# Kernel optimization log

Hardware: AMD Instinct MI355X
Metric: run time of the kernel (lower is better)

The kernel has to match this reference:

```python
import jax, jax.numpy as jnp
import numpy as np

N, E, H, C = 10000, 160000, 7, 64
NEG_SLOPE = 0.2


def setup_inputs() -> dict:
    key = jax.random.key(0)
    ks = iter(jax.random.split(key, 32))
    def w(shape, fan_in):
        return jax.random.normal(next(ks), shape, jnp.float32) * (1.0 / np.sqrt(fan_in))
    inp = {
        "x": jax.random.normal(next(ks), (N, 1024), jnp.float32),
        "edge_index": jax.random.randint(next(ks), (2, E), 0, N, jnp.int64),
        # input MLP 1024->512->256->64
        "W1": w((1024, 512), 1024), "b1": jnp.zeros((512,), jnp.float32),
        "W2": w((512, 256), 512),   "b2": jnp.zeros((256,), jnp.float32),
        "W3": w((256, 64), 256),    "b3": jnp.zeros((64,), jnp.float32),
        # 5 stacked GATv2Conv(64,64,heads=7,concat=False) layers
        "Wl": w((5, 64, H * C), 64), "bl": jnp.zeros((5, H * C), jnp.float32),
        "Wr": w((5, 64, H * C), 64),
        "att": w((5, H, C), C),
        "cbias": jnp.zeros((5, C), jnp.float32),
        # output MLP 64->32->16->9
        "V1": w((64, 32), 64), "c1": jnp.zeros((32,), jnp.float32),
        "V2": w((32, 16), 32), "c2": jnp.zeros((16,), jnp.float32),
        "V3": w((16, 9), 16),  "c3": jnp.zeros((9,), jnp.float32),
    }
    return inp


def _gatv2_conv(x, src, dst, Wl, bl, Wr, att, bias):
    # x: [N,64]; src/dst: [E'] (self-loops already appended)
    xl = (x @ Wl + bl).reshape(N, H, C)   # lin_l (with bias)
    xr = (x @ Wr).reshape(N, H, C)        # lin_r (no bias)
    e = jax.nn.leaky_relu(xl[src] + xr[dst], NEG_SLOPE)      # [E',H,C]
    logits = jnp.einsum('ehc,hc->eh', e, att)                # [E',H]
    m = jax.ops.segment_max(logits, dst, num_segments=N)     # [N,H]
    a = jnp.exp(logits - m[dst])
    s = jax.ops.segment_sum(a, dst, num_segments=N)          # [N,H]
    alpha = a / (s[dst] + 1e-16)                             # ragged softmax per dst node
    out = jax.ops.segment_sum(alpha[:, :, None] * xl[src], dst, num_segments=N)  # [N,H,C]
    return out.mean(axis=1) + bias                           # concat=False -> mean heads


def reference(x, edge_index, W1, b1, W2, b2, W3, b3, Wl, bl, Wr, att, cbias,
              V1, c1, V2, c2, V3, c3):
    # GATv2Conv adds self-loops by default
    loops = jnp.arange(N, dtype=edge_index.dtype)
    src = jnp.concatenate([edge_index[0], loops])
    dst = jnp.concatenate([edge_index[1], loops])

    h = jax.nn.relu(x @ W1 + b1)
    h = jax.nn.relu(h @ W2 + b2)
    h = jax.nn.relu(h @ W3 + b3)
    for l in range(5):
        h = jax.nn.relu(_gatv2_conv(h, src, dst, Wl[l], bl[l], Wr[l], att[l], cbias[l]))
    h = jax.nn.relu(h) @ V1 + c1
    h = jax.nn.relu(h) @ V2 + c2
    h = jax.nn.relu(h) @ V3 + c3
    return jax.nn.log_softmax(h, axis=1)
```

## Files before the change

### kernel.cpp

```cpp
#include <hip/hip_runtime.h>
#include <hip/hip_bf16.h>
#include <math.h>

#define NNODES 10000
#define NEDGES 160000
#define ETOT (NEDGES + NNODES)
#define HEADS 7
#define CH 64
#define HC 448
#define HCP 1024

typedef __attribute__((ext_vector_type(8))) short short8;
typedef __attribute__((ext_vector_type(4))) float floatx4;

__device__ __forceinline__ float bf_lo(unsigned u) {
  return __uint_as_float(u << 16);
}
__device__ __forceinline__ float bf_hi(unsigned u) {
  return __uint_as_float(u & 0xffff0000u);
}
__device__ __forceinline__ short f2bf(float v) {
  return __bfloat16_as_short(__float2bfloat16(v));
}

#define P0 2560000
#define P1 (P0 + 512 * 1024)
#define P2 (P1 + 256 * 512)
#define P3 (P2 + 64 * 256)
#define P4 (P3 + 5 * HCP * 64)
#define P5 (P4 + 5 * HCP)
#define P6 (P5 + NNODES)
#define PTOT P6

__global__ __launch_bounds__(256) void prep_kernel(
    const float* __restrict__ x, short* __restrict__ xb,
    const float* __restrict__ W1, short* __restrict__ W1t,
    const float* __restrict__ W2, short* __restrict__ W2t,
    const float* __restrict__ W3, short* __restrict__ W3t,
    const float* __restrict__ Wl, const float* __restrict__ Wr,
    const float* __restrict__ bl, short* __restrict__ Wgt,
    float* __restrict__ bg, int* __restrict__ cnt) {
  int idx = blockIdx.x * 256 + threadIdx.x;
  if (idx < P0) {
    float4 v = *(const float4*)&x[(size_t)idx * 4];
    short4 o;
    o.x = f2bf(v.x); o.y = f2bf(v.y); o.z = f2bf(v.z); o.w = f2bf(v.w);
    *(short4*)&xb[(size_t)idx * 4] = o;
  } else if (idx < P1) {
    int i = idx - P0;
    int n = i / 1024, k = i % 1024;
    W1t[i] = f2bf(W1[(size_t)k * 512 + n]);
  } else if (idx < P2) {
    int i = idx - P1;
    int n = i / 512, k = i % 512;
    W2t[i] = f2bf(W2[(size_t)k * 256 + n]);
  } else if (idx < P3) {
    int i = idx - P2;
    int n = i / 256, k = i % 256;
    W3t[i] = f2bf(W3[(size_t)k * 64 + n]);
  } else if (idx < P4) {
    int i = idx - P3;
    int l = i / (HCP * 64);
    int rem = i % (HCP * 64);
    int col = rem / 64, k = rem % 64;
    int half = col >> 9;
    int within = col & 511;
    int c = within >> 3, h = within & 7;
    float v = 0.f;
    if (h < 7) {
      const float* W = half ? Wr : Wl;
      v = W[((size_t)l * 64 + k) * HC + h * 64 + c];
    }
    Wgt[i] = f2bf(v);
  } else if (idx < P5) {
    int i = idx - P4;
    int l = i >> 10, col = i & 1023;
    int half = col >> 9, within = col & 511;
    int c = within >> 3, h = within & 7;
    bg[i] = (!half && h < 7) ? bl[(size_t)l * HC + h * 64 + c] : 0.f;
  } else if (idx < P6) {
    cnt[idx - P5] = 1;
  }
}

template <int BM, int BN, int RELU>
__global__ __launch_bounds__(256) void mfma_gemm(
    const short* __restrict__ A, const short* __restrict__ Bt,
    const float* __restrict__ bias, short* __restrict__ C,
    int M, int K, int Nc) {
  __shared__ short As[BM * 64];
  __shared__ short Bs[BN * 64];
  constexpr int MI = BM / 32;
  constexpr int NJ = BN / 32;
  int tid = threadIdx.x;
  int lane = tid & 63, wave = tid >> 6;
  int wm = wave >> 1, wn = wave & 1;
  int row0 = blockIdx.x * BM, col0 = blockIdx.y * BN;
  floatx4 acc[MI][NJ] = {};

  for (int k0 = 0; k0 < K; k0 += 64) {
    #pragma unroll
    for (int i = 0; i < BM / 32; ++i) {
      int c = i * 4 + wave;
      int r = c * 8 + (lane >> 3);
      int k = (lane & 7) * 8;
      int grow = row0 + r;
      if (grow >= M) grow = M - 1;
      __builtin_amdgcn_global_load_lds(
          (const __attribute__((address_space(1))) void*)(A + (size_t)grow * K + k0 + k),
          (__attribute__((address_space(3))) void*)(As + c * 512), 16, 0, 0);
    }
    #pragma unroll
    for (int i = 0; i < BN / 32; ++i) {
      int c = i * 4 + wave;
      int r = c * 8 + (lane >> 3);
      int k = (lane & 7) * 8;
      int gcol = col0 + r;
      if (gcol >= Nc) gcol = Nc - 1;
      __builtin_amdgcn_global_load_lds(
          (const __attribute__((address_space(1))) void*)(Bt + (size_t)gcol * K + k0 + k),
          (__attribute__((address_space(3))) void*)(Bs + c * 512), 16, 0, 0);
    }
    __syncthreads();
    int lr = lane & 15, lq = lane >> 4;
    #pragma unroll
    for (int kk = 0; kk < 64; kk += 32) {
      short8 af[MI], bf[NJ];
      #pragma unroll
      for (int i = 0; i < MI; ++i)
        af[i] = *(const short8*)&As[(wm * (BM / 2) + i * 16 + lr) * 64 + kk + lq * 8];
      #pragma unroll
      for (int j = 0; j < NJ; ++j)
        bf[j] = *(const short8*)&Bs[(wn * (BN / 2) + j * 16 + lr) * 64 + kk + lq * 8];
      #pragma unroll
      for (int i = 0; i < MI; ++i)
        #pragma unroll
        for (int j = 0; j < NJ; ++j)
          acc[i][j] = __builtin_amdgcn_mfma_f32_16x16x32_bf16(
              af[i], bf[j], acc[i][j], 0, 0, 0);
    }
    __syncthreads();
  }

  int lr = lane & 15, lq = lane >> 4;
  #pragma unroll
  for (int j = 0; j < NJ; ++j) {
    int col = col0 + wn * (BN / 2) + j * 16 + lr;
    float bj = bias ? bias[col] : 0.f;
    #pragma unroll
    for (int i = 0; i < MI; ++i) {
      int rbase = row0 + wm * (BM / 2) + i * 16 + lq * 4;
      #pragma unroll
      for (int r = 0; r < 4; ++r) {
        int row = rbase + r;
        if (row < M) {
          float v = acc[i][j][r] + bj;
          if (RELU) v = fmaxf(v, 0.f);
          C[(size_t)row * Nc + col] = f2bf(v);
        }
      }
    }
  }
}

__global__ void hist_kernel(const int* __restrict__ ei, int* __restrict__ cnt) {
  int e = blockIdx.x * 256 + threadIdx.x;
  if (e < NEDGES) atomicAdd(&cnt[ei[NEDGES + e]], 1);
}

__global__ __launch_bounds__(1024) void scan_kernel(
    const int* __restrict__ cnt, int* __restrict__ row_start,
    int* __restrict__ cursor) {
  __shared__ int wsum[16];
  int t = threadIdx.x;
  int lane = t & 63, w = t >> 6;
  int base = t * 10;
  int v[10], s = 0;
  #pragma unroll
  for (int i = 0; i < 10; ++i) {
    v[i] = (base + i < NNODES) ? cnt[base + i] : 0;
    s += v[i];
  }
  int incl = s;
  #pragma unroll
  for (int off = 1; off < 64; off <<= 1) {
    int o = __shfl_up(incl, off, 64);
    if (lane >= off) incl += o;
  }
  if (lane == 63) wsum[w] = incl;
  __syncthreads();
  if (w == 0) {
    int wv = (lane < 16) ? wsum[lane] : 0;
    #pragma unroll
    for (int off = 1; off < 16; off <<= 1) {
      int o = __shfl_up(wv, off, 64);
      if (lane >= off) wv += o;
    }
    if (lane < 16) wsum[lane] = wv;
  }
  __syncthreads();
  int woff = (w > 0) ? wsum[w - 1] : 0;
  int excl = woff + incl - s;
  #pragma unroll
  for (int i = 0; i < 10; ++i) {
    if (base + i < NNODES) {
      row_start[base + i] = excl;
      cursor[base + i] = excl;
    }
    excl += v[i];
  }
  if (t == 1023) row_start[NNODES] = wsum[15];
}

__global__ void scatter_kernel(const int* __restrict__ ei,
                               int* __restrict__ cursor,
                               int* __restrict__ csr_src,
                               int* __restrict__ csr_dst) {
  int t = blockIdx.x * 256 + threadIdx.x;
  if (t < NNODES) {
    int pos = atomicAdd(&cursor[t], 1);
    csr_src[pos] = t;
    csr_dst[pos] = t;
  } else if (t < ETOT) {
    int e = t - NNODES;
    int d = ei[NEDGES + e];
    int pos = atomicAdd(&cursor[d], 1);
    csr_src[pos] = ei[e];
    csr_dst[pos] = d;
  }
}

__global__ __launch_bounds__(256) void edge_logits_kernel(
    const short* __restrict__ xlt, const float* __restrict__ att,
    const int* __restrict__ csr_src, const int* __restrict__ csr_dst,
    float* __restrict__ wbuf) {
  __shared__ float att_s[512];
  for (int i = threadIdx.x; i < 512; i += 256) {
    int c = i >> 3, h = i & 7;
    att_s[i] = (h < 7) ? att[h * 64 + c] : 0.f;
  }
  __syncthreads();
  int lane = threadIdx.x & 63;
  int wid = threadIdx.x >> 6;
  int eo = lane >> 3, cl = lane & 7;
  int e = (blockIdx.x * 4 + wid) * 8 + eo;
  int ec = (e < ETOT) ? e : (ETOT - 1);
  int s = csr_src[ec], d = csr_dst[ec];
  const uint4* xlp = (const uint4*)(xlt + (size_t)s * HCP);
  const uint4* xrp = (const uint4*)(xlt + (size_t)d * HCP + 512);
  float acc[7];
  #pragma unroll
  for (int h = 0; h < 7; ++h) acc[h] = 0.f;
  #pragma unroll
  for (int q = 0; q < 8; ++q) {
    int c = q * 8 + cl;
    uint4 a = xlp[c];
    uint4 b = xrp[c];
    float4 t0 = *(const float4*)&att_s[c * 8];
    float4 t1 = *(const float4*)&att_s[c * 8 + 4];
    float e0 = bf_lo(a.x) + bf_lo(b.x);
    float e1 = bf_hi(a.x) + bf_hi(b.x);
    float e2 = bf_lo(a.y) + bf_lo(b.y);
    float e3 = bf_hi(a.y) + bf_hi(b.y);
    float e4 = bf_lo(a.z) + bf_lo(b.z);
    float e5 = bf_hi(a.z) + bf_hi(b.z);
    float e6 = bf_lo(a.w) + bf_lo(b.w);
    e0 = fmaxf(e0, 0.2f * e0); e1 = fmaxf(e1, 0.2f * e1);
    e2 = fmaxf(e2, 0.2f * e2); e3 = fmaxf(e3, 0.2f * e3);
    e4 = fmaxf(e4, 0.2f * e4); e5 = fmaxf(e5, 0.2f * e5);
    e6 = fmaxf(e6, 0.2f * e6);
    acc[0] += t0.x * e0; acc[1] += t0.y * e1;
    acc[2] += t0.z * e2; acc[3] += t0.w * e3;
    acc[4] += t1.x * e4; acc[5] += t1.y * e5;
    acc[6] += t1.z * e6;
  }
  #pragma unroll
  for (int h = 0; h < 7; ++h) {
    acc[h] += __shfl_xor(acc[h], 1, 64);
    acc[h] += __shfl_xor(acc[h], 2, 64);
    acc[h] += __shfl_xor(acc[h], 4, 64);
  }
  float res = 0.f;
  #pragma unroll
  for (int h = 0; h < 7; ++h) res = (cl == h) ? acc[h] : res;
  float wv = (cl < 7) ? __expf(res) : 0.f;
  if (e < ETOT) wbuf[(size_t)e * 8 + cl] = wv;
}

template <int FINAL>
__global__ __launch_bounds__(256) void gat_agg2_kernel(
    const short* __restrict__ xlt, const float* __restrict__ wbuf,
    const float* __restrict__ cbias, const int* __restrict__ row_start,
    const int* __restrict__ csr_src, short* __restrict__ hout,
    const float* __restrict__ V1, const float* __restrict__ c1,
    const float* __restrict__ V2, const float* __restrict__ c2,
    const float* __restrict__ V3, const float* __restrict__ c3,
    float* __restrict__ out) {
  __shared__ float part[2][14][64];
  __shared__ float hb[2][64], r1[2][32], r2[2][16], z3[2][9];
  int lane = threadIdx.x & 63;
  int wv = threadIdx.x >> 6;
  int nw = wv >> 1;
  int half = wv & 1;
  int n = blockIdx.x * 2 + nw;
  int beg = row_start[n], end = row_start[n + 1];

  float o0 = 0.f, o1 = 0.f, o2 = 0.f, o3 = 0.f, o4 = 0.f, o5 = 0.f, o6 = 0.f;
  float s0 = 0.f, s1 = 0.f, s2 = 0.f, s3 = 0.f, s4 = 0.f, s5 = 0.f, s6 = 0.f;
  #pragma unroll 2
  for (int e = beg + half; e < end; e += 2) {
    int src = csr_src[e];
    float4 wa = *(const float4*)&wbuf[(size_t)e * 8];
    float4 wb = *(const float4*)&wbuf[(size_t)e * 8 + 4];
    uint4 xv = *(const uint4*)(xlt + (size_t)src * HCP + (size_t)lane * 8);
    o0 += wa.x * bf_lo(xv.x);
    o1 += wa.y * bf_hi(xv.x);
    o2 += wa.z * bf_lo(xv.y);
    o3 += wa.w * bf_hi(xv.y);
    o4 += wb.x * bf_lo(xv.z);
    o5 += wb.y * bf_hi(xv.z);
    o6 += wb.z * bf_lo(xv.w);
    s0 += wa.x; s1 += wa.y; s2 += wa.z; s3 += wa.w;
    s4 += wb.x; s5 += wb.y; s6 += wb.z;
  }

  if (half == 1) {
    part[nw][0][lane] = o0;  part[nw][1][lane] = o1;
    part[nw][2][lane] = o2;  part[nw][3][lane] = o3;
    part[nw][4][lane] = o4;  part[nw][5][lane] = o5;
    part[nw][6][lane] = o6;
    part[nw][7][lane] = s0;  part[nw][8][lane] = s1;
    part[nw][9][lane] = s2;  part[nw][10][lane] = s3;
    part[nw][11][lane] = s4; part[nw][12][lane] = s5;
    part[nw][13][lane] = s6;
  }
  __syncthreads();
  if (half == 0) {
    o0 += part[nw][0][lane];  o1 += part[nw][1][lane];
    o2 += part[nw][2][lane];  o3 += part[nw][3][lane];
    o4 += part[nw][4][lane];  o5 += part[nw][5][lane];
    o6 += part[nw][6][lane];
    s0 += part[nw][7][lane];  s1 += part[nw][8][lane];
    s2 += part[nw][9][lane];  s3 += part[nw][10][lane];
    s4 += part[nw][11][lane]; s5 += part[nw][12][lane];
    s6 += part[nw][13][lane];
    float accv = o0 / (s0 + 1e-16f) + o1 / (s1 + 1e-16f) + o2 / (s2 + 1e-16f) +
                 o3 / (s3 + 1e-16f) + o4 / (s4 + 1e-16f) + o5 / (s5 + 1e-16f) +
                 o6 / (s6 + 1e-16f);
    float v = fmaxf(accv * (1.0f / 7.0f) + cbias[lane], 0.f);
    if (!FINAL) {
      hout[(size_t)n * 64 + lane] = f2bf(v);
    } else {
      int t = lane;
      hb[nw][t] = v;
      if (t < 32) {
        float a = c1[t];
        #pragma unroll
        for (int k = 0; k < 64; ++k) a += hb[nw][k] * V1[k * 32 + t];
        r1[nw][t] = fmaxf(a, 0.f);
      }
      if (t < 16) {
        float a = c2[t];
        #pragma unroll
        for (int k = 0; k < 32; ++k) a += r1[nw][k] * V2[k * 16 + t];
        r2[nw][t] = fmaxf(a, 0.f);
      }
      if (t < 9) {
        float a = c3[t];
        #pragma unroll
        for (int k = 0; k < 16; ++k) a += r2[nw][k] * V3[k * 9 + t];
        z3[nw][t] = a;
      }
      if (t < 9) {
        float mx = z3[nw][0];
        #pragma unroll
        for (int k = 1; k < 9; ++k) mx = fmaxf(mx, z3[nw][k]);
        float s = 0.f;
        #pragma unroll
        for (int k = 0; k < 9; ++k) s += __expf(z3[nw][k] - mx);
        out[(size_t)n * 9 + t] = z3[nw][t] - mx - logf(s);
      }
    }
  }
}

extern "C" void kernel_launch(void* const* d_in, const int* in_sizes, int n_in,
                              void* d_out, int out_size, void* d_ws, size_t ws_size,
                              hipStream_t stream) {
  const float* x   = (const float*)d_in[0];
  const int*   ei  = (const int*)d_in[1];
  const float* W1  = (const float*)d_in[2];
  const float* b1  = (const float*)d_in[3];
  const float* W2  = (const float*)d_in[4];
  const float* b2  = (const float*)d_in[5];
  const float* W3  = (const float*)d_in[6];
  const float* b3  = (const float*)d_in[7];
  const float* Wl  = (const float*)d_in[8];
  const float* bl  = (const float*)d_in[9];
  const float* Wr  = (const float*)d_in[10];
  const float* att = (const float*)d_in[11];
  const float* cb  = (const float*)d_in[12];
  const float* V1  = (const float*)d_in[13];
  const float* c1  = (const float*)d_in[14];
  const float* V2  = (const float*)d_in[15];
  const float* c2  = (const float*)d_in[16];
  const float* V3  = (const float*)d_in[17];
  const float* c3  = (const float*)d_in[18];
  float* out = (float*)d_out;

  char* ws = (char*)d_ws;
  size_t off = 0;
  auto alloc = [&](size_t bytes) {
    void* p = ws + off;
    off = (off + bytes + 255) & ~(size_t)255;
    return p;
  };
  char* region0 = (char*)alloc((size_t)NNODES * 1024 * 2 + 1024);
  short* xb  = (short*)region0;
  short* h2  = (short*)region0;
  short* xlt = (short*)region0;
  char* region1 = (char*)alloc((size_t)NNODES * 512 * 2 + 1024);
  short* h1 = (short*)region1;
  short* hA = (short*)region1;
  short* hB = hA + (size_t)NNODES * 64;
  short* W1t = (short*)alloc((size_t)512 * 1024 * 2);
  short* W2t = (short*)alloc((size_t)256 * 512 * 2);
  short* W3t = (short*)alloc((size_t)64 * 256 * 2);
  short* Wgt = (short*)alloc((size_t)5 * HCP * 64 * 2);
  float* bg  = (float*)alloc((size_t)5 * HCP * 4);
  int* cnt       = (int*)alloc((size_t)NNODES * 4);
  int* row_start = (int*)alloc((size_t)(NNODES + 1) * 4);
  int* cursor    = (int*)alloc((size_t)NNODES * 4);
  int* csr_src   = (int*)alloc((size_t)ETOT * 4);
  int* csr_dst   = (int*)alloc((size_t)ETOT * 4);
  float* wbuf    = (float*)alloc((size_t)ETOT * 8 * 4);

  prep_kernel<<<(PTOT + 255) / 256, 256, 0, stream>>>(
      x, xb, W1, W1t, W2, W2t, W3, W3t, Wl, Wr, bl, Wgt, bg, cnt);

  hist_kernel<<<(NEDGES + 255) / 256, 256, 0, stream>>>(ei, cnt);
  scan_kernel<<<1, 1024, 0, stream>>>(cnt, row_start, cursor);
  scatter_kernel<<<(ETOT + 255) / 256, 256, 0, stream>>>(ei, cursor, csr_src, csr_dst);

  mfma_gemm<64, 128, 1><<<dim3(157, 4), 256, 0, stream>>>(
      xb, W1t, b1, h1, NNODES, 1024, 512);
  mfma_gemm<64, 128, 1><<<dim3(157, 2), 256, 0, stream>>>(
      h1, W2t, b2, h2, NNODES, 512, 256);
  mfma_gemm<64, 64, 1><<<dim3(157, 1), 256, 0, stream>>>(
      h2, W3t, b3, hA, NNODES, 256, 64);

  short* hcur = hA;
  short* hnext = hB;
  for (int layer = 0; layer < 5; ++layer) {
    mfma_gemm<128, 128, 0><<<dim3(79, 8), 256, 0, stream>>>(
        hcur, Wgt + (size_t)layer * HCP * 64, bg + (size_t)layer * HCP, xlt,
        NNODES, 64, HCP);
    edge_logits_kernel<<<(ETOT + 31) / 32, 256, 0, stream>>>(
        xlt, att + (size_t)layer * HC, csr_src, csr_dst, wbuf);
    if (layer < 4) {
      gat_agg2_kernel<0><<<5000, 256, 0, stream>>>(
          xlt, wbuf, cb + (size_t)layer * 64, row_start, csr_src, hnext,
          V1, c1, V2, c2, V3, c3, out);
    } else {
      gat_agg2_kernel<1><<<5000, 256, 0, stream>>>(
          xlt, wbuf, cb + (size_t)layer * 64, row_start, csr_src, hnext,
          V1, c1, V2, c2, V3, c3, out);
    }
    short* tmp = hcur; hcur = hnext; hnext = tmp;
  }
}
```

Before: 551.7 us.

## Fuse edge-logit computation into per-node GAT aggregation kernel

Merges the separate edge-logits kernel into the aggregation kernel. Each block now computes exp-logits for its two destination nodes' edges in chunks of up to 128, keeping the xr rows, attention weights and source indices in shared memory. This removes the global wbuf and csr_dst buffers, one kernel launch per layer, and the global write and read of edge weights. In exchange each block now runs the logit phase and the aggregation phase one after the other with barriers between them, and the logit phase may use threads poorly when degrees are low.

```diff
diff --git a/kernel.cpp b/kernel.cpp
--- a/kernel.cpp
+++ b/kernel.cpp
@@ -9,6 +9,7 @@
 #define CH 64
 #define HC 448
 #define HCP 1024
+#define CAP 128
 
 typedef __attribute__((ext_vector_type(8))) short short8;
 typedef __attribute__((ext_vector_type(4))) float floatx4;
@@ -214,128 +215,155 @@
 
 __global__ void scatter_kernel(const int* __restrict__ ei,
                                int* __restrict__ cursor,
-                               int* __restrict__ csr_src,
-                               int* __restrict__ csr_dst) {
+                               int* __restrict__ csr_src) {
   int t = blockIdx.x * 256 + threadIdx.x;
   if (t < NNODES) {
     int pos = atomicAdd(&cursor[t], 1);
     csr_src[pos] = t;
-    csr_dst[pos] = t;
   } else if (t < ETOT) {
     int e = t - NNODES;
     int d = ei[NEDGES + e];
     int pos = atomicAdd(&cursor[d], 1);
     csr_src[pos] = ei[e];
-    csr_dst[pos] = d;
-  }
-}
-
-__global__ __launch_bounds__(256) void edge_logits_kernel(
+  }
+}
+
+template <int FINAL>
+__global__ __launch_bounds__(256) void gat_layer_kernel(
     const short* __restrict__ xlt, const float* __restrict__ att,
-    const int* __restrict__ csr_src, const int* __restrict__ csr_dst,
-    float* __restrict__ wbuf) {
-  __shared__ float att_s[512];
-  for (int i = threadIdx.x; i < 512; i += 256) {
-    int c = i >> 3, h = i & 7;
-    att_s[i] = (h < 7) ? att[h * 64 + c] : 0.f;
-  }
-  __syncthreads();
-  int lane = threadIdx.x & 63;
-  int wid = threadIdx.x >> 6;
-  int eo = lane >> 3, cl = lane & 7;
-  int e = (blockIdx.x * 4 + wid) * 8 + eo;
-  int ec = (e < ETOT) ? e : (ETOT - 1);
-  int s = csr_src[ec], d = csr_dst[ec];
-  const uint4* xlp = (const uint4*)(xlt + (size_t)s * HCP);
-  const uint4* xrp = (const uint4*)(xlt + (size_t)d * HCP + 512);
-  float acc[7];
-  #pragma unroll
-  for (int h = 0; h < 7; ++h) acc[h] = 0.f;
-  #pragma unroll
-  for (int q = 0; q < 8; ++q) {
-    int c = q * 8 + cl;
-    uint4 a = xlp[c];
-    uint4 b = xrp[c];
-    float4 t0 = *(const float4*)&att_s[c * 8];
-    float4 t1 = *(const float4*)&att_s[c * 8 + 4];
-    float e0 = bf_lo(a.x) + bf_lo(b.x);
-    float e1 = bf_hi(a.x) + bf_hi(b.x);
-    float e2 = bf_lo(a.y) + bf_lo(b.y);
-    float e3 = bf_hi(a.y) + bf_hi(b.y);
-    float e4 = bf_lo(a.z) + bf_lo(b.z);
-    float e5 = bf_hi(a.z) + bf_hi(b.z);
-    float e6 = bf_lo(a.w) + bf_lo(b.w);
-    e0 = fmaxf(e0, 0.2f * e0); e1 = fmaxf(e1, 0.2f * e1);
-    e2 = fmaxf(e2, 0.2f * e2); e3 = fmaxf(e3, 0.2f * e3);
-    e4 = fmaxf(e4, 0.2f * e4); e5 = fmaxf(e5, 0.2f * e5);
-    e6 = fmaxf(e6, 0.2f * e6);
-    acc[0] += t0.x * e0; acc[1] += t0.y * e1;
-    acc[2] += t0.z * e2; acc[3] += t0.w * e3;
-    acc[4] += t1.x * e4; acc[5] += t1.y * e5;
-    acc[6] += t1.z * e6;
-  }
-  #pragma unroll
-  for (int h = 0; h < 7; ++h) {
-    acc[h] += __shfl_xor(acc[h], 1, 64);
-    acc[h] += __shfl_xor(acc[h], 2, 64);
-    acc[h] += __shfl_xor(acc[h], 4, 64);
-  }
-  float res = 0.f;
-  #pragma unroll
-  for (int h = 0; h < 7; ++h) res = (cl == h) ? acc[h] : res;
-  float wv = (cl < 7) ? __expf(res) : 0.f;
-  if (e < ETOT) wbuf[(size_t)e * 8 + cl] = wv;
-}
-
-template <int FINAL>
-__global__ __launch_bounds__(256) void gat_agg2_kernel(
-    const short* __restrict__ xlt, const float* __restrict__ wbuf,
     const float* __restrict__ cbias, const int* __restrict__ row_start,
     const int* __restrict__ csr_src, short* __restrict__ hout,
     const float* __restrict__ V1, const float* __restrict__ c1,
     const float* __restrict__ V2, const float* __restrict__ c2,
     const float* __restrict__ V3, const float* __restrict__ c3,
     float* __restrict__ out) {
+  __shared__ float att_s[512];
+  __shared__ short xr_s[2][512];
+  __shared__ float w_s[2][CAP][8];
+  __shared__ int srcs_s[2][CAP];
   __shared__ float part[2][14][64];
   __shared__ float hb[2][64], r1[2][32], r2[2][16], z3[2][9];
-  int lane = threadIdx.x & 63;
-  int wv = threadIdx.x >> 6;
-  int nw = wv >> 1;
-  int half = wv & 1;
-  int n = blockIdx.x * 2 + nw;
-  int beg = row_start[n], end = row_start[n + 1];
+
+  int tid = threadIdx.x;
+  int lane = tid & 63;
+  int wv = tid >> 6;
+  int n0 = blockIdx.x * 2;
+
+  for (int i = tid; i < 512; i += 256) {
+    int c = i >> 3, h = i & 7;
+    att_s[i] = (h < 7) ? att[h * 64 + c] : 0.f;
+  }
+  unsigned* xru = (unsigned*)xr_s;
+  for (int i = tid; i < 512; i += 256) {
+    int node = i >> 8, within = i & 255;
+    xru[i] = *(const unsigned*)(xlt + (size_t)(n0 + node) * HCP + 512 + within * 2);
+  }
+  int beg0 = row_start[n0], beg1 = row_start[n0 + 1], end1 = row_start[n0 + 2];
+  int cnt0 = beg1 - beg0, cnt1 = end1 - beg1;
+  __syncthreads();
+
+  int eo = lane >> 3, cl = lane & 7;
+  int g = wv * 8 + eo;
+  int node_b = wv >> 1, half = wv & 1;
 
   float o0 = 0.f, o1 = 0.f, o2 = 0.f, o3 = 0.f, o4 = 0.f, o5 = 0.f, o6 = 0.f;
   float s0 = 0.f, s1 = 0.f, s2 = 0.f, s3 = 0.f, s4 = 0.f, s5 = 0.f, s6 = 0.f;
-  #pragma unroll 2
-  for (int e = beg + half; e < end; e += 2) {
-    int src = csr_src[e];
-    float4 wa = *(const float4*)&wbuf[(size_t)e * 8];
-    float4 wb = *(const float4*)&wbuf[(size_t)e * 8 + 4];
-    uint4 xv = *(const uint4*)(xlt + (size_t)src * HCP + (size_t)lane * 8);
-    o0 += wa.x * bf_lo(xv.x);
-    o1 += wa.y * bf_hi(xv.x);
-    o2 += wa.z * bf_lo(xv.y);
-    o3 += wa.w * bf_hi(xv.y);
-    o4 += wb.x * bf_lo(xv.z);
-    o5 += wb.y * bf_hi(xv.z);
-    o6 += wb.z * bf_lo(xv.w);
-    s0 += wa.x; s1 += wa.y; s2 += wa.z; s3 += wa.w;
-    s4 += wb.x; s5 += wb.y; s6 += wb.z;
+
+  int cmax = cnt0 > cnt1 ? cnt0 : cnt1;
+  int nch = (cmax + CAP - 1) / CAP;
+  for (int k = 0; k < nch; ++k) {
+    int rem0 = cnt0 - k * CAP;
+    rem0 = rem0 < 0 ? 0 : (rem0 > CAP ? CAP : rem0);
+    int rem1 = cnt1 - k * CAP;
+    rem1 = rem1 < 0 ? 0 : (rem1 > CAP ? CAP : rem1);
+    int tot = rem0 + rem1;
+
+    for (int idx = g; idx < tot; idx += 32) {
+      int node, slot, e;
+      if (idx < rem0) {
+        node = 0; slot = idx; e = beg0 + k * CAP + idx;
+      } else {
+        node = 1; slot = idx - rem0; e = beg1 + k * CAP + idx - rem0;
+      }
+      int src = csr_src[e];
+      const uint4* xlp = (const uint4*)(xlt + (size_t)src * HCP);
+      const uint4* xrp = (const uint4*)&xr_s[node][0];
+      float a0 = 0.f, a1 = 0.f, a2 = 0.f, a3 = 0.f, a4 = 0.f, a5 = 0.f, a6 = 0.f;
+      #pragma unroll
+      for (int q = 0; q < 8; ++q) {
+        int c = q * 8 + cl;
+        uint4 a = xlp[c];
+        uint4 b = xrp[c];
+        float4 t0 = *(const float4*)&att_s[c * 8];
+        float4 t1 = *(const float4*)&att_s[c * 8 + 4];
+        float e0 = bf_lo(a.x) + bf_lo(b.x);
+        float e1 = bf_hi(a.x) + bf_hi(b.x);
+        float e2 = bf_lo(a.y) + bf_lo(b.y);
+        float e3 = bf_hi(a.y) + bf_hi(b.y);
+        float e4 = bf_lo(a.z) + bf_lo(b.z);
+        float e5 = bf_hi(a.z) + bf_hi(b.z);
+        float e6 = bf_lo(a.w) + bf_lo(b.w);
+        e0 = fmaxf(e0, 0.2f * e0); e1 = fmaxf(e1, 0.2f * e1);
+        e2 = fmaxf(e2, 0.2f * e2); e3 = fmaxf(e3, 0.2f * e3);
+        e4 = fmaxf(e4, 0.2f * e4); e5 = fmaxf(e5, 0.2f * e5);
+        e6 = fmaxf(e6, 0.2f * e6);
+        a0 += t0.x * e0; a1 += t0.y * e1;
+        a2 += t0.z * e2; a3 += t0.w * e3;
+        a4 += t1.x * e4; a5 += t1.y * e5;
+        a6 += t1.z * e6;
+      }
+      #pragma unroll
+      for (int st = 1; st <= 4; st <<= 1) {
+        a0 += __shfl_xor(a0, st, 64); a1 += __shfl_xor(a1, st, 64);
+        a2 += __shfl_xor(a2, st, 64); a3 += __shfl_xor(a3, st, 64);
+        a4 += __shfl_xor(a4, st, 64); a5 += __shfl_xor(a5, st, 64);
+        a6 += __shfl_xor(a6, st, 64);
+      }
+      float res = 0.f;
+      res = (cl == 0) ? a0 : res; res = (cl == 1) ? a1 : res;
+      res = (cl == 2) ? a2 : res; res = (cl == 3) ? a3 : res;
+      res = (cl == 4) ? a4 : res; res = (cl == 5) ? a5 : res;
+      res = (cl == 6) ? a6 : res;
+      float wvv = (cl < 7) ? __expf(res) : 0.f;
+      w_s[node][slot][cl] = wvv;
+      if (cl == 0) srcs_s[node][slot] = src;
+    }
+    __syncthreads();
+
+    int rem = node_b == 0 ? rem0 : rem1;
+    #pragma unroll 2
+    for (int sl = half; sl < rem; sl += 2) {
+      int src = srcs_s[node_b][sl];
+      float4 wa = *(const float4*)&w_s[node_b][sl][0];
+      float4 wb = *(const float4*)&w_s[node_b][sl][4];
+      uint4 xv = *(const uint4*)(xlt + (size_t)src * HCP + (size_t)lane * 8);
+      o0 += wa.x * bf_lo(xv.x);
+      o1 += wa.y * bf_hi(xv.x);
+      o2 += wa.z * bf_lo(xv.y);
+      o3 += wa.w * bf_hi(xv.y);
+      o4 += wb.x * bf_lo(xv.z);
+      o5 += wb.y * bf_hi(xv.z);
+      o6 += wb.z * bf_lo(xv.w);
+      s0 += wa.x; s1 += wa.y; s2 += wa.z; s3 += wa.w;
+      s4 += wb.x; s5 += wb.y; s6 += wb.z;
+    }
+    __syncthreads();
   }
 
   if (half == 1) {
-    part[nw][0][lane] = o0;  part[nw][1][lane] = o1;
-    part[nw][2][lane] = o2;  part[nw][3][lane] = o3;
-    part[nw][4][lane] = o4;  part[nw][5][lane] = o5;
-    part[nw][6][lane] = o6;
-    part[nw][7][lane] = s0;  part[nw][8][lane] = s1;
-    part[nw][9][lane] = s2;  part[nw][10][lane] = s3;
-    part[nw][11][lane] = s4; part[nw][12][lane] = s5;
-    part[nw][13][lane] = s6;
+    part[node_b][0][lane] = o0;  part[node_b][1][lane] = o1;
+    part[node_b][2][lane] = o2;  part[node_b][3][lane] = o3;
+    part[node_b][4][lane] = o4;  part[node_b][5][lane] = o5;
+    part[node_b][6][lane] = o6;
+    part[node_b][7][lane] = s0;  part[node_b][8][lane] = s1;
+    part[node_b][9][lane] = s2;  part[node_b][10][lane] = s3;
+    part[node_b][11][lane] = s4; part[node_b][12][lane] = s5;
+    part[node_b][13][lane] = s6;
   }
   __syncthreads();
   if (half == 0) {
+    int nw = node_b;
+    int n = n0 + nw;
     o0 += part[nw][0][lane];  o1 += part[nw][1][lane];
     o2 += part[nw][2][lane];  o3 += part[nw][3][lane];
     o4 += part[nw][4][lane];  o5 += part[nw][5][lane];
@@ -432,15 +460,13 @@
   int* row_start = (int*)alloc((size_t)(NNODES + 1) * 4);
   int* cursor    = (int*)alloc((size_t)NNODES * 4);
   int* csr_src   = (int*)alloc((size_t)ETOT * 4);
-  int* csr_dst   = (int*)alloc((size_t)ETOT * 4);
-  float* wbuf    = (float*)alloc((size_t)ETOT * 8 * 4);
 
   prep_kernel<<<(PTOT + 255) / 256, 256, 0, stream>>>(
       x, xb, W1, W1t, W2, W2t, W3, W3t, Wl, Wr, bl, Wgt, bg, cnt);
 
   hist_kernel<<<(NEDGES + 255) / 256, 256, 0, stream>>>(ei, cnt);
   scan_kernel<<<1, 1024, 0, stream>>>(cnt, row_start, cursor);
-  scatter_kernel<<<(ETOT + 255) / 256, 256, 0, stream>>>(ei, cursor, csr_src, csr_dst);
+  scatter_kernel<<<(ETOT + 255) / 256, 256, 0, stream>>>(ei, cursor, csr_src);
 
   mfma_gemm<64, 128, 1><<<dim3(157, 4), 256, 0, stream>>>(
       xb, W1t, b1, h1, NNODES, 1024, 512);
@@ -455,16 +481,14 @@
     mfma_gemm<128, 128, 0><<<dim3(79, 8), 256, 0, stream>>>(
         hcur, Wgt + (size_t)layer * HCP * 64, bg + (size_t)layer * HCP, xlt,
         NNODES, 64, HCP);
-    edge_logits_kernel<<<(ETOT + 31) / 32, 256, 0, stream>>>(
-        xlt, att + (size_t)layer * HC, csr_src, csr_dst, wbuf);
     if (layer < 4) {
-      gat_agg2_kernel<0><<<5000, 256, 0, stream>>>(
-          xlt, wbuf, cb + (size_t)layer * 64, row_start, csr_src, hnext,
-          V1, c1, V2, c2, V3, c3, out);
+      gat_layer_kernel<0><<<5000, 256, 0, stream>>>(
+          xlt, att + (size_t)layer * HC, cb + (size_t)layer * 64,
+          row_start, csr_src, hnext, V1, c1, V2, c2, V3, c3, out);
     } else {
-      gat_agg2_kernel<1><<<5000, 256, 0, stream>>>(
-          xlt, wbuf, cb + (size_t)layer * 64, row_start, csr_src, hnext,
-          V1, c1, V2, c2, V3, c3, out);
+      gat_layer_kernel<1><<<5000, 256, 0, stream>>>(
+          xlt, att + (size_t)layer * HC, cb + (size_t)layer * 64,
+          row_start, csr_src, hnext, V1, c1, V2, c2, V3, c3, out);
     }
     short* tmp = hcur; hcur = hnext; hnext = tmp;
   }
```

After: 707.2 us. 28.2% more time.
